# Optimization experiments

Measured on AMD Instinct MI355X. Metric: run time of the kernel, lower is better.

The kernel has to match this reference:

```python
import jax, jax.numpy as jnp
import numpy as np

LEAKY_SLOPE = 0.2   # LeakyReLU alpha from __init__
MASK_VAL = -9e15    # matches torch -9000000000000000.0


def setup_inputs() -> dict:
    key = jax.random.key(0)
    ks = jax.random.split(key, 11)
    B, N, L, D = 64, 512, 50, 128
    return {
        "h_locs_l": jax.random.normal(ks[0], (B, L, D), jnp.float32),
        "h_times_l": jax.random.normal(ks[1], (B, L, D), jnp.float32),
        "int_emb": jax.random.normal(ks[2], (B, L, D), jnp.float32),
        "h": jax.random.normal(ks[3], (B, N, D), jnp.float32),
        "adj": jax.random.randint(ks[4], (B, N, N), 0, 5, jnp.int32),
        "wd": jax.random.normal(ks[5], (D, D), jnp.float32),
        "a_0": jax.random.normal(ks[6], (D, 1), jnp.float32),
        "a_1": jax.random.normal(ks[7], (D, 1), jnp.float32),
        "a_2": jax.random.normal(ks[8], (D, 1), jnp.float32),
        "a_3": jax.random.normal(ks[9], (D, 1), jnp.float32),
        "bias": jax.random.normal(ks[10], (D,), jnp.float32),  # declared but unused in forward
    }


def reference(h_locs_l, h_times_l, int_emb, h, adj, wd, a_0, a_1, a_2, a_3, bias):
    # h: [B,N,D]; adj: [B,N,N] int relation types
    # h_ds = mean over concatenated aux sequences, projected by wd -> [B,D]
    h_ds = jnp.mean(jnp.concatenate([h_locs_l, h_times_l, int_emb], axis=1), axis=1) @ wd

    hd = h * h_ds[:, None, :]  # [B,N,D] = h_i * h_ds

    def scores(a):
        # a_input[b,i,j] = h_i*h_ds + h_j*h_ds + h_i*h_j ; e = leakyrelu(a_input @ a)
        # Decompose: rank-1 row/col terms + generalized gram term (never build [B,N,N,D]).
        a = a[:, 0]                                  # [D]
        s = hd @ a                                   # [B,N]
        cross = jnp.einsum('bid,bjd,d->bij', h, h, a)  # [B,N,N]
        e = s[:, :, None] + s[:, None, :] + cross
        return jax.nn.leaky_relu(e, LEAKY_SLOPE)

    e_0, e_1, e_2, e_3 = scores(a_0), scores(a_1), scores(a_2), scores(a_3)

    alpha = jnp.full_like(e_0, MASK_VAL)
    alpha = jnp.where(adj == 1, e_0, alpha)
    alpha = jnp.where(adj == 2, e_1, alpha)
    alpha = jnp.where(adj == 3, e_2, alpha)
    alpha = jnp.where(adj == 4, e_3, alpha)
    alpha = jax.nn.softmax(alpha, axis=-1)
    return jnp.matmul(alpha, h)  # [B,N,D]
```

## Files before the change

kernel.cpp:

```cpp
#include <hip/hip_runtime.h>
#include <hip/hip_bf16.h>
#include <hip/hip_fp16.h>

typedef _Float16 half8 __attribute__((ext_vector_type(8)));
typedef float floatx4 __attribute__((ext_vector_type(4)));
typedef unsigned short u16;
typedef unsigned int u32;
typedef unsigned long long u64;

#define LEAKY 0.2f
#define MASKV -9.0e15f

__global__ __launch_bounds__(256) void k_hds(const float* __restrict__ hl,
                                             const float* __restrict__ ht,
                                             const float* __restrict__ ie,
                                             const float* __restrict__ wd,
                                             float* __restrict__ hds) {
  int b = blockIdx.x, tid = threadIdx.x;
  int d = tid & 127, hh = tid >> 7;
  __shared__ float pa_[2][128];
  __shared__ float ml[128];
  __shared__ float pb_[2][128];
  const size_t base = (size_t)b * 50 * 128 + d;
  float acc = 0.f;
  for (int r = hh * 25; r < hh * 25 + 25; ++r) {
    size_t o = base + (size_t)r * 128;
    acc += hl[o] + ht[o] + ie[o];
  }
  pa_[hh][d] = acc;
  __syncthreads();
  if (hh == 0) ml[d] = (pa_[0][d] + pa_[1][d]) * (1.0f / 150.0f);
  __syncthreads();
  float o = 0.f;
  for (int k = hh * 64; k < hh * 64 + 64; ++k) o = fmaf(ml[k], wd[k * 128 + d], o);
  pb_[hh][d] = o;
  __syncthreads();
  if (hh == 0) hds[b * 128 + d] = pb_[0][d] + pb_[1][d];
}

__global__ __launch_bounds__(256) void k_prep(const float* __restrict__ h,
                                              const float* __restrict__ hds,
                                              const float* __restrict__ a0,
                                              const float* __restrict__ a1,
                                              const float* __restrict__ a2,
                                              const float* __restrict__ a3,
                                              float* __restrict__ s,
                                              u16* __restrict__ h16,
                                              u16* __restrict__ h16T) {
  int b = blockIdx.x >> 3, i0 = (blockIdx.x & 7) * 64;
  int tid = threadIdx.x, w = tid >> 6, l = tid & 63;
  __shared__ u16 tile[64][130];
  int d0 = 2 * l;
  float2 hd2 = *(const float2*)(hds + b * 128 + d0);
  float2 av0 = *(const float2*)(a0 + d0);
  float2 av1 = *(const float2*)(a1 + d0);
  float2 av2 = *(const float2*)(a2 + d0);
  float2 av3 = *(const float2*)(a3 + d0);
  for (int rr = 0; rr < 16; ++rr) {
    int il = rr * 4 + w;
    size_t row = (size_t)b * 512 + i0 + il;
    float2 hv = *(const float2*)(h + row * 128 + d0);
    _Float16 f0 = (_Float16)hv.x, f1 = (_Float16)hv.y;
    u16 u0 = __builtin_bit_cast(u16, f0), u1 = __builtin_bit_cast(u16, f1);
    tile[il][d0] = u0;
    tile[il][d0 + 1] = u1;
    *(u32*)(h16 + row * 128 + d0) = (u32)u0 | ((u32)u1 << 16);
    float t0 = hv.x * hd2.x, t1 = hv.y * hd2.y;
    float p0 = t0 * av0.x + t1 * av0.y;
    float p1 = t0 * av1.x + t1 * av1.y;
    float p2 = t0 * av2.x + t1 * av2.y;
    float p3 = t0 * av3.x + t1 * av3.y;
    for (int off = 32; off >= 1; off >>= 1) {
      p0 += __shfl_xor(p0, off);
      p1 += __shfl_xor(p1, off);
      p2 += __shfl_xor(p2, off);
      p3 += __shfl_xor(p3, off);
    }
    if (l < 4) {
      float pw = (l == 0) ? p0 : (l == 1) ? p1 : (l == 2) ? p2 : p3;
      s[((size_t)l * 64 + b) * 512 + i0 + il] = pw;
    }
  }
  __syncthreads();
  int d = tid >> 1, hf = tid & 1;
  u32 wds[16];
#pragma unroll
  for (int k = 0; k < 16; ++k) {
    u32 lo = tile[32 * hf + 2 * k][d];
    u32 hi = tile[32 * hf + 2 * k + 1][d];
    wds[k] = lo | (hi << 16);
  }
  uint4* dst = (uint4*)(h16T + ((size_t)b * 128 + d) * 512 + i0 + 32 * hf);
  dst[0] = make_uint4(wds[0], wds[1], wds[2], wds[3]);
  dst[1] = make_uint4(wds[4], wds[5], wds[6], wds[7]);
  dst[2] = make_uint4(wds[8], wds[9], wds[10], wds[11]);
  dst[3] = make_uint4(wds[12], wds[13], wds[14], wds[15]);
}

__global__ __launch_bounds__(256, 2) void k_attn(const u16* __restrict__ h16,
                                                 const u16* __restrict__ h16T,
                                                 const float* __restrict__ s,
                                                 const int* __restrict__ adj,
                                                 const float* __restrict__ a0,
                                                 const float* __restrict__ a1,
                                                 const float* __restrict__ a2,
                                                 const float* __restrict__ a3,
                                                 float* __restrict__ out) {
  int bid = blockIdx.x;
  int wg = (bid & 7) * 256 + (bid >> 3);
  int b = wg >> 5, i0r = (wg & 31) * 16;
  int tid = threadIdx.x, jq = tid >> 6, l = tid & 63;
  int l15 = l & 15, l4 = l >> 4;

  __shared__ u16 a16[4][128];
  __shared__ float s_lds[4][512];
  __shared__ u16 pbuf[4][16][72];
  __shared__ float mrg[3][16][132];
  __shared__ float mml[3][16][2];

  const size_t hb16 = (size_t)b * 512 * 128;
  const size_t hTb = (size_t)b * 128 * 512;

  u32 ct[2][4];
#pragma unroll
  for (int t = 0; t < 2; ++t)
#pragma unroll
    for (int e = 0; e < 4; ++e) {
      u32 v = 0;
      const int* ap = adj + ((size_t)(b * 512 + i0r + 4 * l4 + e)) * 512 + jq * 128 + t * 64 + l15;
#pragma unroll
      for (int C = 0; C < 4; ++C) {
        int av = ap[16 * C];
        if (av > 0) v |= (1u << (4 * (av - 1) + C));
      }
      ct[t][e] = v;
    }

  half8 hf[4];
#pragma unroll
  for (int ks = 0; ks < 4; ++ks)
    hf[ks] = *(const half8*)(h16 + hb16 + (size_t)(i0r + l15) * 128 + ks * 32 + 8 * l4);

  if (tid < 128) {
    a16[0][tid] = __builtin_bit_cast(u16, (_Float16)a0[tid]);
    a16[1][tid] = __builtin_bit_cast(u16, (_Float16)a1[tid]);
    a16[2][tid] = __builtin_bit_cast(u16, (_Float16)a2[tid]);
    a16[3][tid] = __builtin_bit_cast(u16, (_Float16)a3[tid]);
  }
#pragma unroll
  for (int p = 0; p < 2; ++p) {
    int cid = p * 256 + tid;
    int hd = cid >> 7, i4 = (cid & 127) * 4;
    *(float4*)&s_lds[hd][i4] = *(const float4*)(s + ((size_t)hd * 64 + b) * 512 + i4);
  }
  __syncthreads();

  float m[4], lsum[4];
#pragma unroll
  for (int e = 0; e < 4; ++e) { m[e] = MASKV; lsum[e] = 0.f; }
  floatx4 pv[8];
#pragma unroll
  for (int dt = 0; dt < 8; ++dt) pv[dt] = (floatx4){0.f, 0.f, 0.f, 0.f};

  auto load_kfa = [&](int j0, half8* dst) {
#pragma unroll
    for (int ks = 0; ks < 4; ++ks)
#pragma unroll
      for (int C = 0; C < 4; ++C)
        dst[ks * 4 + C] = *(const half8*)(h16 + hb16 + (size_t)(j0 + 16 * C + l15) * 128 + ks * 32 + 8 * l4);
  };
  auto load_vba = [&](int j0, half8* dst) {
#pragma unroll
    for (int ks2 = 0; ks2 < 2; ++ks2)
#pragma unroll
      for (int dt = 0; dt < 8; ++dt)
        dst[ks2 * 8 + dt] = *(const half8*)(h16T + hTb + (size_t)(16 * dt + l15) * 512 + j0 + ks2 * 32 + 8 * l4);
  };
  auto qk_select = [&](const u32* ctv, const half8* kfa, int j0, float x[4][4]) {
#pragma unroll
    for (int C = 0; C < 4; ++C)
#pragma unroll
      for (int e = 0; e < 4; ++e) x[C][e] = MASKV;
#pragma unroll
    for (int hd = 0; hd < 4; ++hd) {
      float sjh[4], sih[4];
#pragma unroll
      for (int C = 0; C < 4; ++C) sjh[C] = s_lds[hd][j0 + 16 * C + l15];
#pragma unroll
      for (int e = 0; e < 4; ++e) sih[e] = s_lds[hd][i0r + 4 * l4 + e];
      floatx4 qk[4];
#pragma unroll
      for (int C = 0; C < 4; ++C) qk[C] = (floatx4){0.f, 0.f, 0.f, 0.f};
      __builtin_amdgcn_s_setprio(1);
#pragma unroll
      for (int ks = 0; ks < 4; ++ks) {
        half8 af = *(const half8*)&a16[hd][ks * 32 + 8 * l4];
        half8 q = hf[ks] * af;
#pragma unroll
        for (int C = 0; C < 4; ++C)
          qk[C] = __builtin_amdgcn_mfma_f32_16x16x32_f16(q, kfa[ks * 4 + C], qk[C], 0, 0, 0);
      }
      __builtin_amdgcn_s_setprio(0);
#pragma unroll
      for (int e = 0; e < 4; ++e) {
#pragma unroll
        for (int C = 0; C < 4; ++C) {
          if ((ctv[e] >> (4 * hd + C)) & 1) {
            float v = qk[C][e] + sih[e] + sjh[C];
            x[C][e] = (v > 0.f) ? v : LEAKY * v;
          }
        }
      }
    }
  };
  auto softmax_store = [&](float x[4][4]) {
#pragma unroll
    for (int e = 0; e < 4; ++e) {
      float tmax = fmaxf(fmaxf(x[0][e], x[1][e]), fmaxf(x[2][e], x[3][e]));
      tmax = fmaxf(tmax, __shfl_xor(tmax, 1));
      tmax = fmaxf(tmax, __shfl_xor(tmax, 2));
      tmax = fmaxf(tmax, __shfl_xor(tmax, 4));
      tmax = fmaxf(tmax, __shfl_xor(tmax, 8));
      float mn = fmaxf(m[e], tmax);
      float sc = __expf(m[e] - mn);
      float p0 = __expf(x[0][e] - mn);
      float p1 = __expf(x[1][e] - mn);
      float p2 = __expf(x[2][e] - mn);
      float p3 = __expf(x[3][e] - mn);
      float ls = (p0 + p1) + (p2 + p3);
      ls += __shfl_xor(ls, 1);
      ls += __shfl_xor(ls, 2);
      ls += __shfl_xor(ls, 4);
      ls += __shfl_xor(ls, 8);
      lsum[e] = lsum[e] * sc + ls;
      m[e] = mn;
#pragma unroll
      for (int dt = 0; dt < 8; ++dt) pv[dt][e] *= sc;
      int r = 4 * l4 + e;
      pbuf[jq][r][0 + l15] = __builtin_bit_cast(u16, (_Float16)p0);
      pbuf[jq][r][16 + l15] = __builtin_bit_cast(u16, (_Float16)p1);
      pbuf[jq][r][32 + l15] = __builtin_bit_cast(u16, (_Float16)p2);
      pbuf[jq][r][48 + l15] = __builtin_bit_cast(u16, (_Float16)p3);
    }
  };
  auto pv_mfma = [&](const half8* vba) {
    __builtin_amdgcn_s_setprio(1);
#pragma unroll
    for (int ks2 = 0; ks2 < 2; ++ks2) {
      half8 pa = *(const half8*)((const char*)&pbuf[jq][0][0] + l15 * 144 + ks2 * 64 + l4 * 16);
#pragma unroll
      for (int dt = 0; dt < 8; ++dt)
        pv[dt] = __builtin_amdgcn_mfma_f32_16x16x32_f16(pa, vba[ks2 * 8 + dt], pv[dt], 0, 0, 0);
    }
    __builtin_amdgcn_s_setprio(0);
  };

  const int j0a = jq * 128, j0b = jq * 128 + 64;
  half8 kfa0[16], kfa1[16], vba[16];
  float x[4][4];

  load_kfa(j0a, kfa0);
  qk_select(&ct[0][0], kfa0, j0a, x);
  load_vba(j0a, vba);
  load_kfa(j0b, kfa1);
  softmax_store(x);
  asm volatile("s_waitcnt lgkmcnt(0)" ::: "memory");
  __builtin_amdgcn_sched_barrier(0);
  pv_mfma(vba);

  qk_select(&ct[1][0], kfa1, j0b, x);
  load_vba(j0b, vba);
  softmax_store(x);
  asm volatile("s_waitcnt lgkmcnt(0)" ::: "memory");
  __builtin_amdgcn_sched_barrier(0);
  pv_mfma(vba);

  if (jq != 0) {
#pragma unroll
    for (int dt = 0; dt < 8; ++dt)
#pragma unroll
      for (int e = 0; e < 4; ++e)
        mrg[jq - 1][4 * l4 + e][16 * dt + l15] = pv[dt][e];
    if (l15 == 0) {
#pragma unroll
      for (int e = 0; e < 4; ++e) {
        mml[jq - 1][4 * l4 + e][0] = m[e];
        mml[jq - 1][4 * l4 + e][1] = lsum[e];
      }
    }
  }
  __syncthreads();
  if (jq == 0) {
    float wq[4][3], inv[4];
#pragma unroll
    for (int e = 0; e < 4; ++e) {
      int r = 4 * l4 + e;
      float M = m[e];
#pragma unroll
      for (int q = 0; q < 3; ++q) M = fmaxf(M, mml[q][r][0]);
      float w0 = __expf(m[e] - M);
      float L = lsum[e] * w0;
#pragma unroll
      for (int q = 0; q < 3; ++q) {
        wq[e][q] = __expf(mml[q][r][0] - M);
        L += mml[q][r][1] * wq[e][q];
      }
      inv[e] = 1.0f / L;
      wq[e][0] *= inv[e]; wq[e][1] *= inv[e]; wq[e][2] *= inv[e];
      inv[e] *= w0;
    }
#pragma unroll
    for (int dt = 0; dt < 8; ++dt)
#pragma unroll
      for (int e = 0; e < 4; ++e) {
        int r = 4 * l4 + e;
        float o = pv[dt][e] * inv[e];
#pragma unroll
        for (int q = 0; q < 3; ++q) o += mrg[q][r][16 * dt + l15] * wq[e][q];
        out[((size_t)b * 512 + i0r + r) * 128 + 16 * dt + l15] = o;
      }
  }
}

extern "C" void kernel_launch(void* const* d_in, const int* in_sizes, int n_in,
                              void* d_out, int out_size, void* d_ws, size_t ws_size,
                              hipStream_t stream) {
  const float* hl = (const float*)d_in[0];
  const float* ht = (const float*)d_in[1];
  const float* ie = (const float*)d_in[2];
  const float* h  = (const float*)d_in[3];
  const int* adj  = (const int*)d_in[4];
  const float* wd = (const float*)d_in[5];
  const float* a0 = (const float*)d_in[6];
  const float* a1 = (const float*)d_in[7];
  const float* a2 = (const float*)d_in[8];
  const float* a3 = (const float*)d_in[9];

  float* hds  = (float*)d_ws;
  float* s    = (float*)((char*)d_ws + 32768);
  u16* h16    = (u16*)((char*)d_ws + 557056);
  u16* h16T   = (u16*)((char*)d_ws + 8945664);
  float* o    = (float*)d_out;

  k_hds<<<64, 256, 0, stream>>>(hl, ht, ie, wd, hds);
  k_prep<<<512, 256, 0, stream>>>(h, hds, a0, a1, a2, a3, s, h16, h16T);
  k_attn<<<2048, 256, 0, stream>>>(h16, h16T, s, adj, a0, a1, a2, a3, o);
}
```

Before: 107.8 us.

## Reuse single K fragment buffer and specialize first softmax tile

Drops the second K-fragment register array so both 64-column tiles share one buffer, loading K and V for each tile just before its QK step instead of prefetching the next tile's K. Adds a first-tile softmax that skips the running-max rescale and the initialisation of m and lsum. The intent is to lower VGPR pressure and remove redundant exp and rescale work, at the cost of less overlap between global loads and MFMA compute.

```diff
diff --git a/kernel.cpp b/kernel.cpp
--- a/kernel.cpp
+++ b/kernel.cpp
@@ -156,8 +156,6 @@
   __syncthreads();
 
   float m[4], lsum[4];
-#pragma unroll
-  for (int e = 0; e < 4; ++e) { m[e] = MASKV; lsum[e] = 0.f; }
   floatx4 pv[8];
 #pragma unroll
   for (int dt = 0; dt < 8; ++dt) pv[dt] = (floatx4){0.f, 0.f, 0.f, 0.f};
@@ -211,6 +209,32 @@
           }
         }
       }
+    }
+  };
+  auto softmax_first = [&](float x[4][4]) {
+#pragma unroll
+    for (int e = 0; e < 4; ++e) {
+      float tmax = fmaxf(fmaxf(x[0][e], x[1][e]), fmaxf(x[2][e], x[3][e]));
+      tmax = fmaxf(tmax, __shfl_xor(tmax, 1));
+      tmax = fmaxf(tmax, __shfl_xor(tmax, 2));
+      tmax = fmaxf(tmax, __shfl_xor(tmax, 4));
+      tmax = fmaxf(tmax, __shfl_xor(tmax, 8));
+      float p0 = __expf(x[0][e] - tmax);
+      float p1 = __expf(x[1][e] - tmax);
+      float p2 = __expf(x[2][e] - tmax);
+      float p3 = __expf(x[3][e] - tmax);
+      float ls = (p0 + p1) + (p2 + p3);
+      ls += __shfl_xor(ls, 1);
+      ls += __shfl_xor(ls, 2);
+      ls += __shfl_xor(ls, 4);
+      ls += __shfl_xor(ls, 8);
+      lsum[e] = ls;
+      m[e] = tmax;
+      int r = 4 * l4 + e;
+      pbuf[jq][r][0 + l15] = __builtin_bit_cast(u16, (_Float16)p0);
+      pbuf[jq][r][16 + l15] = __builtin_bit_cast(u16, (_Float16)p1);
+      pbuf[jq][r][32 + l15] = __builtin_bit_cast(u16, (_Float16)p2);
+      pbuf[jq][r][48 + l15] = __builtin_bit_cast(u16, (_Float16)p3);
     }
   };
   auto softmax_store = [&](float x[4][4]) {
@@ -256,20 +280,20 @@
   };
 
   const int j0a = jq * 128, j0b = jq * 128 + 64;
-  half8 kfa0[16], kfa1[16], vba[16];
+  half8 kfa[16], vba[16];
   float x[4][4];
 
-  load_kfa(j0a, kfa0);
-  qk_select(&ct[0][0], kfa0, j0a, x);
+  load_kfa(j0a, kfa);
   load_vba(j0a, vba);
-  load_kfa(j0b, kfa1);
-  softmax_store(x);
+  qk_select(&ct[0][0], kfa, j0a, x);
+  softmax_first(x);
   asm volatile("s_waitcnt lgkmcnt(0)" ::: "memory");
   __builtin_amdgcn_sched_barrier(0);
   pv_mfma(vba);
 
-  qk_select(&ct[1][0], kfa1, j0b, x);
+  load_kfa(j0b, kfa);
   load_vba(j0b, vba);
+  qk_select(&ct[1][0], kfa, j0b, x);
   softmax_store(x);
   asm volatile("s_waitcnt lgkmcnt(0)" ::: "memory");
   __builtin_amdgcn_sched_barrier(0);
```

Measured after the change: 109.6 us. Within noise of the previous version (+1.6%).

## Transpose score MFMA to keep probabilities in registers, drop LDS P buffer

Applied to the files above, without the earlier changes.

Swaps the MFMA operand order so each lane holds the scores of one query row across 16 keys. Softmax then reduces with two cross-lane shuffles instead of four, and the fp16 probabilities feed straight into a 16x16x16 PV MFMA from registers, removing the LDS round trip through pbuf. adj is now read as int4 vectors and compared directly rather than packed into bitmasks. The final merge of the four partial outputs is spread across all warps with float4 LDS reads and writes. The trade-offs are twice as many narrower PV MFMAs, half4 V loads, one K fragment buffer reused instead of a prefetched second one, and a larger merge scratch area.

```diff
diff --git a/kernel.cpp b/kernel.cpp
--- a/kernel.cpp
+++ b/kernel.cpp
@@ -3,6 +3,7 @@
 #include <hip/hip_fp16.h>
 
 typedef _Float16 half8 __attribute__((ext_vector_type(8)));
+typedef _Float16 half4 __attribute__((ext_vector_type(4)));
 typedef float floatx4 __attribute__((ext_vector_type(4)));
 typedef unsigned short u16;
 typedef unsigned int u32;
@@ -114,27 +115,18 @@
 
   __shared__ u16 a16[4][128];
   __shared__ float s_lds[4][512];
-  __shared__ u16 pbuf[4][16][72];
-  __shared__ float mrg[3][16][132];
-  __shared__ float mml[3][16][2];
+  __shared__ float mrg[4][16][132];
+  __shared__ float mml[4][16][2];
 
   const size_t hb16 = (size_t)b * 512 * 128;
   const size_t hTb = (size_t)b * 128 * 512;
-
-  u32 ct[2][4];
-#pragma unroll
-  for (int t = 0; t < 2; ++t)
-#pragma unroll
-    for (int e = 0; e < 4; ++e) {
-      u32 v = 0;
-      const int* ap = adj + ((size_t)(b * 512 + i0r + 4 * l4 + e)) * 512 + jq * 128 + t * 64 + l15;
-#pragma unroll
-      for (int C = 0; C < 4; ++C) {
-        int av = ap[16 * C];
-        if (av > 0) v |= (1u << (4 * (av - 1) + C));
-      }
-      ct[t][e] = v;
-    }
+  const int j0a = jq * 128, j0b = jq * 128 + 64;
+  const int* adjrow = adj + ((size_t)(b * 512 + i0r + l15)) * 512;
+
+  int4 av0[4];
+#pragma unroll
+  for (int C = 0; C < 4; ++C)
+    av0[C] = *(const int4*)(adjrow + j0a + 16 * C + 4 * l4);
 
   half8 hf[4];
 #pragma unroll
@@ -155,9 +147,7 @@
   }
   __syncthreads();
 
-  float m[4], lsum[4];
-#pragma unroll
-  for (int e = 0; e < 4; ++e) { m[e] = MASKV; lsum[e] = 0.f; }
+  float m = MASKV, lsum = 0.f;
   floatx4 pv[8];
 #pragma unroll
   for (int dt = 0; dt < 8; ++dt) pv[dt] = (floatx4){0.f, 0.f, 0.f, 0.f};
@@ -169,25 +159,24 @@
       for (int C = 0; C < 4; ++C)
         dst[ks * 4 + C] = *(const half8*)(h16 + hb16 + (size_t)(j0 + 16 * C + l15) * 128 + ks * 32 + 8 * l4);
   };
-  auto load_vba = [&](int j0, half8* dst) {
-#pragma unroll
-    for (int ks2 = 0; ks2 < 2; ++ks2)
-#pragma unroll
-      for (int dt = 0; dt < 8; ++dt)
-        dst[ks2 * 8 + dt] = *(const half8*)(h16T + hTb + (size_t)(16 * dt + l15) * 512 + j0 + ks2 * 32 + 8 * l4);
-  };
-  auto qk_select = [&](const u32* ctv, const half8* kfa, int j0, float x[4][4]) {
+  auto load_vba = [&](int j0, half4* dst) {
+#pragma unroll
+    for (int dt = 0; dt < 8; ++dt)
+#pragma unroll
+      for (int C = 0; C < 4; ++C)
+        dst[dt * 4 + C] = *(const half4*)(h16T + hTb + (size_t)(16 * dt + l15) * 512 + j0 + 16 * C + 4 * l4);
+  };
+  auto qk_select = [&](const int4* av, const half8* kfa, int j0, float x[4][4]) {
 #pragma unroll
     for (int C = 0; C < 4; ++C)
 #pragma unroll
       for (int e = 0; e < 4; ++e) x[C][e] = MASKV;
 #pragma unroll
     for (int hd = 0; hd < 4; ++hd) {
-      float sjh[4], sih[4];
-#pragma unroll
-      for (int C = 0; C < 4; ++C) sjh[C] = s_lds[hd][j0 + 16 * C + l15];
-#pragma unroll
-      for (int e = 0; e < 4; ++e) sih[e] = s_lds[hd][i0r + 4 * l4 + e];
+      float si_h = s_lds[hd][i0r + l15];
+      float4 sj[4];
+#pragma unroll
+      for (int C = 0; C < 4; ++C) sj[C] = *(const float4*)&s_lds[hd][j0 + 16 * C + 4 * l4];
       floatx4 qk[4];
 #pragma unroll
       for (int C = 0; C < 4; ++C) qk[C] = (floatx4){0.f, 0.f, 0.f, 0.f};
@@ -198,127 +187,117 @@
         half8 q = hf[ks] * af;
 #pragma unroll
         for (int C = 0; C < 4; ++C)
-          qk[C] = __builtin_amdgcn_mfma_f32_16x16x32_f16(q, kfa[ks * 4 + C], qk[C], 0, 0, 0);
+          qk[C] = __builtin_amdgcn_mfma_f32_16x16x32_f16(kfa[ks * 4 + C], q, qk[C], 0, 0, 0);
       }
       __builtin_amdgcn_s_setprio(0);
 #pragma unroll
-      for (int e = 0; e < 4; ++e) {
-#pragma unroll
-        for (int C = 0; C < 4; ++C) {
-          if ((ctv[e] >> (4 * hd + C)) & 1) {
-            float v = qk[C][e] + sih[e] + sjh[C];
+      for (int C = 0; C < 4; ++C) {
+        int va[4] = {av[C].x, av[C].y, av[C].z, av[C].w};
+#pragma unroll
+        for (int e = 0; e < 4; ++e) {
+          if (va[e] == hd + 1) {
+            float v = qk[C][e] + si_h + ((const float*)&sj[C])[e];
             x[C][e] = (v > 0.f) ? v : LEAKY * v;
           }
         }
       }
     }
   };
-  auto softmax_store = [&](float x[4][4]) {
-#pragma unroll
-    for (int e = 0; e < 4; ++e) {
-      float tmax = fmaxf(fmaxf(x[0][e], x[1][e]), fmaxf(x[2][e], x[3][e]));
-      tmax = fmaxf(tmax, __shfl_xor(tmax, 1));
-      tmax = fmaxf(tmax, __shfl_xor(tmax, 2));
-      tmax = fmaxf(tmax, __shfl_xor(tmax, 4));
-      tmax = fmaxf(tmax, __shfl_xor(tmax, 8));
-      float mn = fmaxf(m[e], tmax);
-      float sc = __expf(m[e] - mn);
-      float p0 = __expf(x[0][e] - mn);
-      float p1 = __expf(x[1][e] - mn);
-      float p2 = __expf(x[2][e] - mn);
-      float p3 = __expf(x[3][e] - mn);
-      float ls = (p0 + p1) + (p2 + p3);
-      ls += __shfl_xor(ls, 1);
-      ls += __shfl_xor(ls, 2);
-      ls += __shfl_xor(ls, 4);
-      ls += __shfl_xor(ls, 8);
-      lsum[e] = lsum[e] * sc + ls;
-      m[e] = mn;
-#pragma unroll
-      for (int dt = 0; dt < 8; ++dt) pv[dt][e] *= sc;
-      int r = 4 * l4 + e;
-      pbuf[jq][r][0 + l15] = __builtin_bit_cast(u16, (_Float16)p0);
-      pbuf[jq][r][16 + l15] = __builtin_bit_cast(u16, (_Float16)p1);
-      pbuf[jq][r][32 + l15] = __builtin_bit_cast(u16, (_Float16)p2);
-      pbuf[jq][r][48 + l15] = __builtin_bit_cast(u16, (_Float16)p3);
-    }
-  };
-  auto pv_mfma = [&](const half8* vba) {
+  auto softmax_pack = [&](const float x[4][4], bool first, half4* pb) {
+    float tmax = x[0][0];
+#pragma unroll
+    for (int C = 0; C < 4; ++C)
+#pragma unroll
+      for (int e = 0; e < 4; ++e) tmax = fmaxf(tmax, x[C][e]);
+    tmax = fmaxf(tmax, __shfl_xor(tmax, 16));
+    tmax = fmaxf(tmax, __shfl_xor(tmax, 32));
+    float mn = first ? tmax : fmaxf(m, tmax);
+    float p[4][4], ls = 0.f;
+#pragma unroll
+    for (int C = 0; C < 4; ++C)
+#pragma unroll
+      for (int e = 0; e < 4; ++e) {
+        p[C][e] = __expf(x[C][e] - mn);
+        ls += p[C][e];
+      }
+    ls += __shfl_xor(ls, 16);
+    ls += __shfl_xor(ls, 32);
+    if (first) {
+      lsum = ls;
+    } else {
+      float sc = __expf(m - mn);
+      lsum = lsum * sc + ls;
+#pragma unroll
+      for (int dt = 0; dt < 8; ++dt) pv[dt] *= sc;
+    }
+    m = mn;
+#pragma unroll
+    for (int C = 0; C < 4; ++C) {
+      half4 t;
+      t[0] = (_Float16)p[C][0]; t[1] = (_Float16)p[C][1];
+      t[2] = (_Float16)p[C][2]; t[3] = (_Float16)p[C][3];
+      pb[C] = t;
+    }
+  };
+  auto pv_mfma = [&](const half4* vba, const half4* pb) {
     __builtin_amdgcn_s_setprio(1);
 #pragma unroll
-    for (int ks2 = 0; ks2 < 2; ++ks2) {
-      half8 pa = *(const half8*)((const char*)&pbuf[jq][0][0] + l15 * 144 + ks2 * 64 + l4 * 16);
-#pragma unroll
-      for (int dt = 0; dt < 8; ++dt)
-        pv[dt] = __builtin_amdgcn_mfma_f32_16x16x32_f16(pa, vba[ks2 * 8 + dt], pv[dt], 0, 0, 0);
-    }
+    for (int dt = 0; dt < 8; ++dt)
+#pragma unroll
+      for (int C = 0; C < 4; ++C)
+        pv[dt] = __builtin_amdgcn_mfma_f32_16x16x16f16(vba[dt * 4 + C], pb[C], pv[dt], 0, 0, 0);
     __builtin_amdgcn_s_setprio(0);
   };
 
-  const int j0a = jq * 128, j0b = jq * 128 + 64;
-  half8 kfa0[16], kfa1[16], vba[16];
+  half8 kfa[16];
+  half4 vba[32], pb[4];
   float x[4][4];
 
-  load_kfa(j0a, kfa0);
-  qk_select(&ct[0][0], kfa0, j0a, x);
+  load_kfa(j0a, kfa);
+  qk_select(av0, kfa, j0a, x);
   load_vba(j0a, vba);
-  load_kfa(j0b, kfa1);
-  softmax_store(x);
-  asm volatile("s_waitcnt lgkmcnt(0)" ::: "memory");
-  __builtin_amdgcn_sched_barrier(0);
-  pv_mfma(vba);
-
-  qk_select(&ct[1][0], kfa1, j0b, x);
+  int4 av1[4];
+#pragma unroll
+  for (int C = 0; C < 4; ++C)
+    av1[C] = *(const int4*)(adjrow + j0b + 16 * C + 4 * l4);
+  softmax_pack(x, true, pb);
+  pv_mfma(vba, pb);
+
+  load_kfa(j0b, kfa);
+  qk_select(av1, kfa, j0b, x);
   load_vba(j0b, vba);
-  softmax_store(x);
-  asm volatile("s_waitcnt lgkmcnt(0)" ::: "memory");
-  __builtin_amdgcn_sched_barrier(0);
-  pv_mfma(vba);
-
-  if (jq != 0) {
-#pragma unroll
-    for (int dt = 0; dt < 8; ++dt)
-#pragma unroll
-      for (int e = 0; e < 4; ++e)
-        mrg[jq - 1][4 * l4 + e][16 * dt + l15] = pv[dt][e];
-    if (l15 == 0) {
-#pragma unroll
-      for (int e = 0; e < 4; ++e) {
-        mml[jq - 1][4 * l4 + e][0] = m[e];
-        mml[jq - 1][4 * l4 + e][1] = lsum[e];
-      }
-    }
-  }
-  __syncthreads();
-  if (jq == 0) {
-    float wq[4][3], inv[4];
-#pragma unroll
-    for (int e = 0; e < 4; ++e) {
-      int r = 4 * l4 + e;
-      float M = m[e];
-#pragma unroll
-      for (int q = 0; q < 3; ++q) M = fmaxf(M, mml[q][r][0]);
-      float w0 = __expf(m[e] - M);
-      float L = lsum[e] * w0;
-#pragma unroll
-      for (int q = 0; q < 3; ++q) {
-        wq[e][q] = __expf(mml[q][r][0] - M);
-        L += mml[q][r][1] * wq[e][q];
-      }
-      inv[e] = 1.0f / L;
-      wq[e][0] *= inv[e]; wq[e][1] *= inv[e]; wq[e][2] *= inv[e];
-      inv[e] *= w0;
-    }
-#pragma unroll
-    for (int dt = 0; dt < 8; ++dt)
-#pragma unroll
-      for (int e = 0; e < 4; ++e) {
-        int r = 4 * l4 + e;
-        float o = pv[dt][e] * inv[e];
-#pragma unroll
-        for (int q = 0; q < 3; ++q) o += mrg[q][r][16 * dt + l15] * wq[e][q];
-        out[((size_t)b * 512 + i0r + r) * 128 + 16 * dt + l15] = o;
-      }
+  softmax_pack(x, false, pb);
+  pv_mfma(vba, pb);
+
+#pragma unroll
+  for (int dt = 0; dt < 8; ++dt)
+    *(floatx4*)&mrg[jq][l15][16 * dt + 4 * l4] = pv[dt];
+  if (l4 == 0) {
+    mml[jq][l15][0] = m;
+    mml[jq][l15][1] = lsum;
+  }
+  __syncthreads();
+
+#pragma unroll
+  for (int p2 = 0; p2 < 2; ++p2) {
+    int i = (tid >> 5) + 8 * p2;
+    int dc = (tid & 31) * 4;
+    float m0 = mml[0][i][0], m1 = mml[1][i][0], m2 = mml[2][i][0], m3 = mml[3][i][0];
+    float M = fmaxf(fmaxf(m0, m1), fmaxf(m2, m3));
+    float w0 = __expf(m0 - M), w1 = __expf(m1 - M), w2 = __expf(m2 - M), w3 = __expf(m3 - M);
+    float L = mml[0][i][1] * w0 + mml[1][i][1] * w1 + mml[2][i][1] * w2 + mml[3][i][1] * w3;
+    float inv = 1.0f / L;
+    w0 *= inv; w1 *= inv; w2 *= inv; w3 *= inv;
+    float4 v0 = *(float4*)&mrg[0][i][dc];
+    float4 v1 = *(float4*)&mrg[1][i][dc];
+    float4 v2 = *(float4*)&mrg[2][i][dc];
+    float4 v3 = *(float4*)&mrg[3][i][dc];
+    float4 o;
+    o.x = v0.x * w0 + v1.x * w1 + v2.x * w2 + v3.x * w3;
+    o.y = v0.y * w0 + v1.y * w1 + v2.y * w2 + v3.y * w3;
+    o.z = v0.z * w0 + v1.z * w1 + v2.z * w2 + v3.z * w3;
+    o.w = v0.w * w0 + v1.w * w1 + v2.w * w2 + v3.w * w3;
+    *(float4*)(out + ((size_t)b * 512 + i0r + i) * 128 + dc) = o;
   }
 }
 
```

Measured after the change: 127.8 us. +18.6%, slower.
